# Performance work log

Measured on AMD Instinct MI355X. Metric: run time of the kernel, lower is better.

The kernel has to match this reference:

```python
import jax, jax.numpy as jnp
import numpy as np

EPS = 1e-5

def binarize(x):
    # straight-through-estimator sign binarization (identity gradient),
    # matching the torch .data-mutation trick in BinarizeConv2d/BinarizeLinear
    return x + jax.lax.stop_gradient(jnp.sign(x) - x)

def conv3x3(x, w, b):
    # NCHW conv, stride 1, padding 1, binarized weights, float bias
    y = jax.lax.conv_general_dilated(x, binarize(w), window_strides=(1, 1),
                                     padding=((1, 1), (1, 1)),
                                     dimension_numbers=('NCHW', 'OIHW', 'NCHW'))
    return y + b[None, :, None, None]

def maxpool2(x):
    return jax.lax.reduce_window(x, -jnp.inf, jax.lax.max,
                                 (1, 1, 2, 2), (1, 1, 2, 2), 'VALID')

def bn2d(x, g, b):
    # training-mode batchnorm (batch statistics)
    m = jnp.mean(x, axis=(0, 2, 3), keepdims=True)
    v = jnp.var(x, axis=(0, 2, 3), keepdims=True)
    return (x - m) * jax.lax.rsqrt(v + EPS) * g[None, :, None, None] + b[None, :, None, None]

def bn1d(x, g, b):
    m = jnp.mean(x, axis=0)
    v = jnp.var(x, axis=0)
    return (x - m) * jax.lax.rsqrt(v + EPS) * g + b

def htanh(x):
    return jnp.clip(x, -1.0, 1.0)


def setup_inputs() -> dict:
    key = jax.random.key(0)
    ks = jax.random.split(key, 16)
    B = 1024
    inp = {
        'x':   jax.random.normal(ks[0], (B, 1, 28, 28), jnp.float32),
        'w1':  jax.random.normal(ks[1], (48, 1, 3, 3), jnp.float32) * 0.1,
        'b1':  jnp.zeros((48,), jnp.float32),
        'g1':  jnp.ones((48,), jnp.float32),  'be1': jnp.zeros((48,), jnp.float32),
        'w2':  jax.random.normal(ks[2], (128, 48, 3, 3), jnp.float32) * 0.05,
        'b2':  jnp.zeros((128,), jnp.float32),
        'g2':  jnp.ones((128,), jnp.float32), 'be2': jnp.zeros((128,), jnp.float32),
        'w3':  jax.random.normal(ks[3], (256, 128, 3, 3), jnp.float32) * 0.03,
        'b3':  jnp.zeros((256,), jnp.float32),
        'g3':  jnp.ones((256,), jnp.float32), 'be3': jnp.zeros((256,), jnp.float32),
        'wf1': jax.random.normal(ks[4], (2048, 256 * 7 * 7), jnp.float32) * 0.01,
        'bf1': jnp.zeros((2048,), jnp.float32),
        'g4':  jnp.ones((2048,), jnp.float32), 'be4': jnp.zeros((2048,), jnp.float32),
        'wf2': jax.random.normal(ks[5], (10, 2048), jnp.float32) * 0.02,
        'bf2': jnp.zeros((10,), jnp.float32),
    }
    return inp


def reference(x, w1, b1, g1, be1, w2, b2, g2, be2, w3, b3, g3, be3,
              wf1, bf1, g4, be4, wf2, bf2):
    # features
    h = conv3x3(binarize(x), w1, b1)          # [B,48,28,28] (input binarized: C=1 != 3)
    h = maxpool2(h)                            # [B,48,14,14]
    h = htanh(bn2d(h, g1, be1))
    h = conv3x3(binarize(h), w2, b2)          # [B,128,14,14]
    h = htanh(bn2d(h, g2, be2))
    h = conv3x3(binarize(h), w3, b3)          # [B,256,14,14]
    h = maxpool2(h)                            # [B,256,7,7]
    h = htanh(bn2d(h, g3, be3))
    # classifier
    h = h.reshape(-1, 256 * 7 * 7)
    h = binarize(h) @ binarize(wf1).T + bf1    # [B,2048]
    h = htanh(bn1d(h, g4, be4))
    # Dropout(0.5) is identity in eval mode
    h = h @ wf2.T + bf2                        # [B,10]
    return jax.nn.log_softmax(h, axis=1)
```

## Files before the change

### kernel.cpp

```cpp
#include <hip/hip_runtime.h>
#include <math.h>

typedef __attribute__((ext_vector_type(8))) short short8;
typedef __attribute__((ext_vector_type(4))) float f32x4;
typedef unsigned short ushort_t;

#define B_    1024
#define EPSV  1e-5

__device__ __forceinline__ float sgn(float v){ return (v>0.f)?1.f:((v<0.f)?-1.f:0.f); }
__device__ __forceinline__ ushort_t sgnbits(float v){ return (v>0.f)?(ushort_t)0x3F80:((v<0.f)?(ushort_t)0xBF80:(ushort_t)0); }

__global__ __launch_bounds__(256) void k_conv1_pool(const float* __restrict__ x,
                                                    const float* __restrict__ w1,
                                                    float* __restrict__ p1){
  int idx = blockIdx.x*256 + threadIdx.x;
  if (idx >= B_*196*64) return;
  int c = idx & 63;
  int p = (idx >> 6) % 196;
  int b = (idx >> 6) / 196;
  if (c >= 48){ p1[idx] = 0.f; return; }
  int y = p/14, xq = p - y*14;
  const float* xb = x + (size_t)b*784;
  float w[9];
#pragma unroll
  for (int k=0;k<9;k++) w[k] = sgn(w1[c*9+k]);
  float sx[4][4];
#pragma unroll
  for (int dy=0; dy<4; dy++){
    int iy = 2*y-1+dy;
#pragma unroll
    for (int dx=0; dx<4; dx++){
      int ix = 2*xq-1+dx;
      sx[dy][dx] = (iy>=0 && iy<28 && ix>=0 && ix<28) ? sgn(xb[iy*28+ix]) : 0.f;
    }
  }
  float best = -1e30f;
#pragma unroll
  for (int py=0;py<2;py++)
#pragma unroll
    for (int px=0;px<2;px++){
      float acc = 0.f;
#pragma unroll
      for (int ky=0;ky<3;ky++)
#pragma unroll
        for (int kx=0;kx<3;kx++)
          acc += sx[py+ky][px+kx]*w[ky*3+kx];
      best = fmaxf(best, acc);
    }
  p1[idx] = best;
}

__global__ __launch_bounds__(256) void k_stats_cols(const float* __restrict__ src,
                                                    double* __restrict__ sum,
                                                    double* __restrict__ sumsq,
                                                    int C, long rows){
  int c = blockIdx.x*256 + threadIdx.x;
  if (c >= C) return;
  double a=0.0, a2=0.0;
  for (long r = blockIdx.y; r < rows; r += gridDim.y){
    double v = (double)src[r*(long)C + c];
    a += v; a2 += v*v;
  }
  atomicAdd(&sum[c], a); atomicAdd(&sumsq[c], a2);
}

__global__ __launch_bounds__(256) void k_stats_cf(const float* __restrict__ src,
                                                  double* __restrict__ sum,
                                                  double* __restrict__ sumsq,
                                                  int Bn, int C, int S){
  int c = blockIdx.x;
  long NS = (long)Bn*S;
  double a=0.0, a2=0.0;
  long stride = (long)gridDim.y*blockDim.x;
  for (long i = (long)blockIdx.y*blockDim.x + threadIdx.x; i < NS; i += stride){
    long b = i / S, s = i - b*S;
    double v = (double)src[((size_t)b*C + c)*S + s];
    a += v; a2 += v*v;
  }
  __shared__ double rs[256], rs2[256];
  rs[threadIdx.x]=a; rs2[threadIdx.x]=a2;
  __syncthreads();
  for (int off=128; off>0; off>>=1){
    if (threadIdx.x < off){ rs[threadIdx.x]+=rs[threadIdx.x+off]; rs2[threadIdx.x]+=rs2[threadIdx.x+off]; }
    __syncthreads();
  }
  if (threadIdx.x==0){ atomicAdd(&sum[c], rs[0]); atomicAdd(&sumsq[c], rs2[0]); }
}

__global__ void k_bnparams(const double* __restrict__ sum, const double* __restrict__ sumsq,
                           const float* __restrict__ g, const float* __restrict__ be,
                           float* __restrict__ scale, float* __restrict__ shift,
                           int C, int validC, double invN){
  int c = blockIdx.x*blockDim.x + threadIdx.x;
  if (c >= C) return;
  if (c >= validC){ scale[c]=0.f; shift[c]=0.f; return; }
  double m   = sum[c]*invN;
  double var = sumsq[c]*invN - m*m;
  double s   = (double)g[c] / sqrt(var + EPSV);
  scale[c] = (float)s;
  shift[c] = (float)((double)be[c] - m*s);
}

__global__ __launch_bounds__(256) void k_norm_sign(const float* __restrict__ src,
                                                   ushort_t* __restrict__ dst,
                                                   const float* __restrict__ scale,
                                                   const float* __restrict__ shift,
                                                   int C, int S, int total){
  int i = blockIdx.x*256 + threadIdx.x;
  if (i >= total) return;
  int c = (i / S) % C;
  float v = fmaf(src[i], scale[c], shift[c]);
  dst[i] = sgnbits(v);
}

__global__ __launch_bounds__(256) void k_norm_htanh(float* __restrict__ buf,
                                                    const float* __restrict__ scale,
                                                    const float* __restrict__ shift,
                                                    int C, int total){
  int i = blockIdx.x*256 + threadIdx.x;
  if (i >= total) return;
  int c = i % C;
  float v = fmaf(buf[i], scale[c], shift[c]);
  buf[i] = fminf(fmaxf(v,-1.f),1.f);
}

__global__ __launch_bounds__(256) void k_prep_w2(const float* __restrict__ w2, ushort_t* __restrict__ out){
  int idx = blockIdx.x*256 + threadIdx.x;
  if (idx >= 128*576) return;
  int oc = idx / 576, r = idx - oc*576;
  int kk = r >> 6, ic = r & 63;
  out[idx] = (ic < 48) ? sgnbits(w2[oc*432 + ic*9 + kk]) : (ushort_t)0;
}
__global__ __launch_bounds__(256) void k_prep_w3(const float* __restrict__ w3, ushort_t* __restrict__ out){
  int idx = blockIdx.x*256 + threadIdx.x;
  if (idx >= 256*1152) return;
  int oc = idx / 1152, r = idx - oc*1152;
  int kk = r >> 7, ic = r & 127;
  out[idx] = sgnbits(w3[oc*1152 + ic*9 + kk]);
}
__global__ __launch_bounds__(256) void k_prep_wf1(const float* __restrict__ wf1, ushort_t* __restrict__ out){
  int idx = blockIdx.x*256 + threadIdx.x;
  if (idx >= 2048*12544/4) return;
  const float4 v = *reinterpret_cast<const float4*>(&wf1[(size_t)idx*4]);
  ushort4 o;
  o.x = sgnbits(v.x); o.y = sgnbits(v.y); o.z = sgnbits(v.z); o.w = sgnbits(v.w);
  *reinterpret_cast<ushort4*>(&out[(size_t)idx*4]) = o;
}

__global__ __launch_bounds__(256,2) void k_conv2_mfma(const ushort_t* __restrict__ a1,
                                                      const ushort_t* __restrict__ w2b,
                                                      float* __restrict__ c2){
  __shared__ ushort_t sIn[256*64];
  __shared__ ushort_t sW[2][64*40];
  int ocb = blockIdx.x*64;
  int b   = blockIdx.y;
  int tid = threadIdx.x;
  {
    const uint4* src4 = reinterpret_cast<const uint4*>(a1 + (size_t)b*196*64);
    for (int i = tid; i < 2048; i += 256){
      int px = i >> 3, ch = i & 7;
      int py = px >> 4, pxx = px & 15;
      uint4 v = make_uint4(0u,0u,0u,0u);
      if (py>=1 && py<=14 && pxx>=1 && pxx<=14)
        v = src4[((py-1)*14 + (pxx-1))*8 + ch];
      *reinterpret_cast<uint4*>(&sIn[px*64 + ((ch ^ (px & 7))<<3)]) = v;
    }
  }
  const uint4* wsrc = reinterpret_cast<const uint4*>(w2b);
  int ocS = ocb + (tid>>2), kcS = tid & 3;
  *reinterpret_cast<uint4*>(&sW[0][(tid>>2)*40 + kcS*8]) = wsrc[(size_t)ocS*72 + kcS];
  __syncthreads();

  int lane = tid & 63, wave = tid >> 6;
  int rA = lane & 15, kch = lane >> 4;
  f32x4 acc[4][4];
#pragma unroll
  for (int t=0;t<4;t++)
#pragma unroll
    for (int n=0;n<4;n++) acc[t][n] = (f32x4){0.f,0.f,0.f,0.f};

  for (int s = 0; s < 18; ++s){
    int cur = s & 1;
    uint4 wpre;
    if (s < 17) wpre = wsrc[(size_t)ocS*72 + (s+1)*4 + kcS];
    short8 bF[4];
#pragma unroll
    for (int n=0;n<4;n++)
      bF[n] = *reinterpret_cast<const short8*>(&sW[cur][(n*16+rA)*40 + kch*8]);
    int kk9 = s >> 1;
    int ky = kk9/3, kx = kk9 - ky*3;
    int chbase = ((s & 1) << 2) + kch;
#pragma unroll
    for (int t=0;t<4;t++){
      int m = t*4 + wave;
      if (m < 13){
        int r = m*16 + rA;
        int rc = r < 196 ? r : 195;
        int y = rc/14, x = rc - y*14;
        int px = (y+ky)*16 + (x+kx);
        short8 aF = *reinterpret_cast<const short8*>(&sIn[px*64 + ((chbase ^ (px&7))<<3)]);
#pragma unroll
        for (int n=0;n<4;n++)
          acc[t][n] = __builtin_amdgcn_mfma_f32_16x16x32_bf16(aF, bF[n], acc[t][n], 0,0,0);
      }
    }
    if (s < 17) *reinterpret_cast<uint4*>(&sW[cur^1][(tid>>2)*40 + kcS*8]) = wpre;
    __syncthreads();
  }
  int colL = lane & 15, rg = lane >> 4;
#pragma unroll
  for (int t=0;t<4;t++){
    int m = t*4 + wave;
    if (m < 13){
#pragma unroll
      for (int n=0;n<4;n++)
#pragma unroll
        for (int j=0;j<4;j++){
          int r = m*16 + rg*4 + j;
          if (r < 196)
            c2[((size_t)b*196 + r)*128 + ocb + n*16 + colL] = acc[t][n][j];
        }
    }
  }
}

__global__ __launch_bounds__(256,2) void k_conv3_mfma_pool(const ushort_t* __restrict__ a2,
                                                           const ushort_t* __restrict__ w3b,
                                                           float* __restrict__ p3){
  __shared__ ushort_t sIn[256*128];
  __shared__ ushort_t sW[2][64*40];
  int ocb = blockIdx.x*64;
  int b   = blockIdx.y;
  int tid = threadIdx.x;
  {
    const uint4* src4 = reinterpret_cast<const uint4*>(a2 + (size_t)b*196*128);
    for (int i = tid; i < 4096; i += 256){
      int px = i >> 4, ch = i & 15;
      int py = px >> 4, pxx = px & 15;
      uint4 v = make_uint4(0u,0u,0u,0u);
      if (py>=1 && py<=14 && pxx>=1 && pxx<=14)
        v = src4[((py-1)*14 + (pxx-1))*16 + ch];
      *reinterpret_cast<uint4*>(&sIn[px*128 + ((ch ^ (px & 15))<<3)]) = v;
    }
  }
  const uint4* wsrc = reinterpret_cast<const uint4*>(w3b);
  int ocS = ocb + (tid>>2), kcS = tid & 3;
  *reinterpret_cast<uint4*>(&sW[0][(tid>>2)*40 + kcS*8]) = wsrc[(size_t)ocS*144 + kcS];
  __syncthreads();

  int lane = tid & 63, wave = tid >> 6;
  int rA = lane & 15, kch = lane >> 4;
  f32x4 acc[4][4];
#pragma unroll
  for (int t=0;t<4;t++)
#pragma unroll
    for (int n=0;n<4;n++) acc[t][n] = (f32x4){0.f,0.f,0.f,0.f};

  for (int s = 0; s < 36; ++s){
    int cur = s & 1;
    uint4 wpre;
    if (s < 35) wpre = wsrc[(size_t)ocS*144 + (s+1)*4 + kcS];
    short8 bF[4];
#pragma unroll
    for (int n=0;n<4;n++)
      bF[n] = *reinterpret_cast<const short8*>(&sW[cur][(n*16+rA)*40 + kch*8]);
    int kk9 = s >> 2;
    int ky = kk9/3, kx = kk9 - ky*3;
    int chbase = ((s & 3) << 2) + kch;
#pragma unroll
    for (int t=0;t<4;t++){
      int m = t*4 + wave;
      if (m < 13){
        int r = m*16 + rA;
        int rc = r < 196 ? r : 195;
        int y = rc/14, x = rc - y*14;
        int px = (y+ky)*16 + (x+kx);
        short8 aF = *reinterpret_cast<const short8*>(&sIn[px*128 + ((chbase ^ (px&15))<<3)]);
#pragma unroll
        for (int n=0;n<4;n++)
          acc[t][n] = __builtin_amdgcn_mfma_f32_16x16x32_bf16(aF, bF[n], acc[t][n], 0,0,0);
      }
    }
    if (s < 35) *reinterpret_cast<uint4*>(&sW[cur^1][(tid>>2)*40 + kcS*8]) = wpre;
    __syncthreads();
  }
  float* sPool = reinterpret_cast<float*>(sIn);
  int colL = lane & 15, rg = lane >> 4;
#pragma unroll
  for (int t=0;t<4;t++){
    int m = t*4 + wave;
    if (m < 13){
#pragma unroll
      for (int n=0;n<4;n++)
#pragma unroll
        for (int j=0;j<4;j++){
          int r = m*16 + rg*4 + j;
          if (r < 196) sPool[(n*16+colL)*212 + r] = acc[t][n][j];
        }
    }
  }
  __syncthreads();
  for (int i = tid; i < 64*49; i += 256){
    int oc = i/49, cell = i - oc*49;
    int cy = cell/7, cx = cell - cy*7;
    const float* rp = &sPool[oc*212 + cy*28 + cx*2];
    float m0 = fmaxf(rp[0],  rp[1]);
    float m1 = fmaxf(rp[14], rp[15]);
    p3[((size_t)b*256 + ocb + oc)*49 + cell] = fmaxf(m0, m1);
  }
}

__global__ __launch_bounds__(256) void k_fc1_mfma(const ushort_t* __restrict__ A,
                                                  const ushort_t* __restrict__ Bw,
                                                  float* __restrict__ f1){
  __shared__ ushort_t As[2][64*40];
  __shared__ ushort_t Bs[2][128*40];
  int bn = blockIdx.x*128, bm = blockIdx.y*64;
  int tid = threadIdx.x;
  int rS = tid >> 2, kcS = tid & 3;
  {
    *reinterpret_cast<uint4*>(&As[0][rS*40 + kcS*8]) =
      *reinterpret_cast<const uint4*>(&A[(size_t)(bm+rS)*12544 + kcS*8]);
    *reinterpret_cast<uint4*>(&Bs[0][rS*40 + kcS*8]) =
      *reinterpret_cast<const uint4*>(&Bw[(size_t)(bn+rS)*12544 + kcS*8]);
    *reinterpret_cast<uint4*>(&Bs[0][(64+rS)*40 + kcS*8]) =
      *reinterpret_cast<const uint4*>(&Bw[(size_t)(bn+64+rS)*12544 + kcS*8]);
  }
  __syncthreads();
  int lane = tid & 63, wave = tid >> 6;
  int rA = lane & 15, kch = lane >> 4;
  int mtb = (wave & 1)*2, ntb = (wave >> 1)*4;
  f32x4 acc[2][4];
#pragma unroll
  for (int i=0;i<2;i++)
#pragma unroll
    for (int n=0;n<4;n++) acc[i][n] = (f32x4){0.f,0.f,0.f,0.f};

  for (int s = 0; s < 392; ++s){
    int cur = s & 1;
    uint4 pa, pb0, pb1;
    if (s < 391){
      size_t k0 = (size_t)(s+1)*32 + kcS*8;
      pa  = *reinterpret_cast<const uint4*>(&A [(size_t)(bm+rS)*12544 + k0]);
      pb0 = *reinterpret_cast<const uint4*>(&Bw[(size_t)(bn+rS)*12544 + k0]);
      pb1 = *reinterpret_cast<const uint4*>(&Bw[(size_t)(bn+64+rS)*12544 + k0]);
    }
    short8 aF[2], bF[4];
#pragma unroll
    for (int i=0;i<2;i++)
      aF[i] = *reinterpret_cast<const short8*>(&As[cur][((mtb+i)*16+rA)*40 + kch*8]);
#pragma unroll
    for (int n=0;n<4;n++)
      bF[n] = *reinterpret_cast<const short8*>(&Bs[cur][((ntb+n)*16+rA)*40 + kch*8]);
#pragma unroll
    for (int i=0;i<2;i++)
#pragma unroll
      for (int n=0;n<4;n++)
        acc[i][n] = __builtin_amdgcn_mfma_f32_16x16x32_bf16(aF[i], bF[n], acc[i][n], 0,0,0);
    if (s < 391){
      *reinterpret_cast<uint4*>(&As[cur^1][rS*40 + kcS*8]) = pa;
      *reinterpret_cast<uint4*>(&Bs[cur^1][rS*40 + kcS*8]) = pb0;
      *reinterpret_cast<uint4*>(&Bs[cur^1][(64+rS)*40 + kcS*8]) = pb1;
    }
    __syncthreads();
  }
  int colL = lane & 15, rg = lane >> 4;
#pragma unroll
  for (int i=0;i<2;i++)
#pragma unroll
    for (int n=0;n<4;n++)
#pragma unroll
      for (int j=0;j<4;j++){
        int r = bm + (mtb+i)*16 + rg*4 + j;
        int col = bn + (ntb+n)*16 + colL;
        f1[(size_t)r*2048 + col] = acc[i][n][j];
      }
}

__global__ __launch_bounds__(256) void k_fc2_lsm(const float* __restrict__ h,
                                                 const float* __restrict__ W,
                                                 const float* __restrict__ bias,
                                                 float* __restrict__ out){
  int b = blockIdx.x;
  const float* hb = h + (size_t)b*2048;
  float acc[10];
#pragma unroll
  for (int o=0;o<10;o++) acc[o]=0.f;
  for (int k=threadIdx.x; k<2048; k+=256){
    float v = hb[k];
#pragma unroll
    for (int o=0;o<10;o++) acc[o] += v*W[o*2048+k];
  }
  __shared__ float red[4][10];
  int wv = threadIdx.x>>6, lanev = threadIdx.x&63;
#pragma unroll
  for (int o=0;o<10;o++){
    float r = acc[o];
    for (int off=32; off>0; off>>=1) r += __shfl_down(r, off);
    if (lanev==0) red[wv][o]=r;
  }
  __syncthreads();
  if (threadIdx.x==0){
    float lg[10], mx=-1e30f;
#pragma unroll
    for (int o=0;o<10;o++){ lg[o]=red[0][o]+red[1][o]+red[2][o]+red[3][o]+bias[o]; mx=fmaxf(mx,lg[o]); }
    float se=0.f;
#pragma unroll
    for (int o=0;o<10;o++) se += expf(lg[o]-mx);
    float lse = mx + logf(se);
#pragma unroll
    for (int o=0;o<10;o++) out[(size_t)b*10+o] = lg[o]-lse;
  }
}

extern "C" void kernel_launch(void* const* d_in, const int* in_sizes, int n_in,
                              void* d_out, int out_size, void* d_ws, size_t ws_size,
                              hipStream_t stream){
  (void)in_sizes; (void)n_in; (void)out_size; (void)ws_size;
  const float* x   = (const float*)d_in[0];
  const float* w1  = (const float*)d_in[1];
  const float* g1  = (const float*)d_in[3];
  const float* be1 = (const float*)d_in[4];
  const float* w2  = (const float*)d_in[5];
  const float* g2  = (const float*)d_in[7];
  const float* be2 = (const float*)d_in[8];
  const float* w3  = (const float*)d_in[9];
  const float* g3  = (const float*)d_in[11];
  const float* be3 = (const float*)d_in[12];
  const float* wf1 = (const float*)d_in[13];
  const float* g4  = (const float*)d_in[15];
  const float* be4 = (const float*)d_in[16];
  const float* wf2 = (const float*)d_in[17];
  const float* bf2 = (const float*)d_in[18];
  float* out = (float*)d_out;

  char* W = (char*)d_ws;
  double* sum   = (double*)W;
  double* sumsq = sum + 2048;
  float*  scale = (float*)(W + 32768);
  float*  shift = scale + 2048;
  float*    p1   = (float*)   (W + 65536);
  float*    c2   = (float*)   (W + 65536);
  float*    p3   = (float*)   (W + 65536);
  ushort_t* a3   = (ushort_t*)(W + 51445760);
  ushort_t* wf1b = (ushort_t*)(W + 77135872);
  ushort_t* a1   = (ushort_t*)(W + 102825984);
  ushort_t* w2b  = (ushort_t*)(W + 128516096);
  ushort_t* a2   = (ushort_t*)(W + 128663552);
  ushort_t* w3b  = (ushort_t*)(W + 180043776);
  float*    f1   = (float*)   (W + 180633600);

  k_conv1_pool<<<50176, 256, 0, stream>>>(x, w1, p1);
  hipMemsetAsync(sum, 0, 32768, stream);
  k_stats_cols<<<dim3(1,512), 256, 0, stream>>>(p1, sum, sumsq, 64, 200704L);
  k_bnparams<<<1, 256, 0, stream>>>(sum, sumsq, g1, be1, scale, shift, 64, 48, 1.0/200704.0);
  k_norm_sign<<<50176, 256, 0, stream>>>(p1, a1, scale, shift, 64, 1, 12845056);
  k_prep_w2<<<288, 256, 0, stream>>>(w2, w2b);
  k_conv2_mfma<<<dim3(2, B_), 256, 0, stream>>>(a1, w2b, c2);
  hipMemsetAsync(sum, 0, 32768, stream);
  k_stats_cols<<<dim3(1,512), 256, 0, stream>>>(c2, sum, sumsq, 128, 200704L);
  k_bnparams<<<1, 256, 0, stream>>>(sum, sumsq, g2, be2, scale, shift, 128, 128, 1.0/200704.0);
  k_norm_sign<<<100352, 256, 0, stream>>>(c2, a2, scale, shift, 128, 1, 25690112);
  k_prep_wf1<<<25088, 256, 0, stream>>>(wf1, wf1b);
  k_prep_w3<<<1152, 256, 0, stream>>>(w3, w3b);
  k_conv3_mfma_pool<<<dim3(4, B_), 256, 0, stream>>>(a2, w3b, p3);
  hipMemsetAsync(sum, 0, 32768, stream);
  k_stats_cf<<<dim3(256,16), 256, 0, stream>>>(p3, sum, sumsq, B_, 256, 49);
  k_bnparams<<<1, 256, 0, stream>>>(sum, sumsq, g3, be3, scale, shift, 256, 256, 1.0/50176.0);
  k_norm_sign<<<50176, 256, 0, stream>>>(p3, a3, scale, shift, 256, 49, 12845056);
  k_fc1_mfma<<<dim3(16,16), 256, 0, stream>>>(a3, wf1b, f1);
  hipMemsetAsync(sum, 0, 32768, stream);
  k_stats_cols<<<dim3(8,64), 256, 0, stream>>>(f1, sum, sumsq, 2048, 1024L);
  k_bnparams<<<8, 256, 0, stream>>>(sum, sumsq, g4, be4, scale, shift, 2048, 2048, 1.0/1024.0);
  k_norm_htanh<<<8192, 256, 0, stream>>>(f1, scale, shift, 2048, 2097152);
  k_fc2_lsm<<<B_, 256, 0, stream>>>(f1, wf2, bf2, out);
}
```

Measured before the change: 1.084 ms.

## Fuse BN statistics into conv/fc epilogues and widen MFMA tiles

Conv2, conv3 and fc1 now accumulate per-channel sum and sum-of-squares in their epilogues and write per-block partials. A small reduce kernel combines them, replacing the separate passes that re-read c2, p3 and f1. Conv2 computes all 128 output channels per block, and conv3 uses 128-channel tiles that stage input channels in two halves of shared memory. The fc1 K-step doubles to 64 with swizzled shared layouts, and the first BN stats kernel uses a 4-row-per-block layout. Partial sums are fp32 before the double reduction, which slightly changes precision, and the larger accumulator tiles raise register pressure.

```diff
diff --git a/kernel.cpp b/kernel.cpp
--- a/kernel.cpp
+++ b/kernel.cpp
@@ -10,6 +10,9 @@
 
 __device__ __forceinline__ float sgn(float v){ return (v>0.f)?1.f:((v<0.f)?-1.f:0.f); }
 __device__ __forceinline__ ushort_t sgnbits(float v){ return (v>0.f)?(ushort_t)0x3F80:((v<0.f)?(ushort_t)0xBF80:(ushort_t)0); }
+
+#define SWZW(o,c) ( ((o)<<6) ^ ((((c) ^ ((o)&7)) & 7) << 4) )
+#define SWZF(o,c) ( ((o)<<7) + ((((c) ^ ((o)&7)) & 7) << 4) )
 
 __global__ __launch_bounds__(256) void k_conv1_pool(const float* __restrict__ x,
                                                     const float* __restrict__ w1,
@@ -51,41 +54,42 @@
   p1[idx] = best;
 }
 
-__global__ __launch_bounds__(256) void k_stats_cols(const float* __restrict__ src,
+__global__ __launch_bounds__(256) void k_stats_cl64(const float* __restrict__ src,
                                                     double* __restrict__ sum,
                                                     double* __restrict__ sumsq,
-                                                    int C, long rows){
+                                                    long rows){
+  int c = threadIdx.x & 63, sl = threadIdx.x >> 6;
+  double a=0.0, q=0.0;
+  long stride = (long)gridDim.y*4;
+  for (long r = (long)blockIdx.y*4 + sl; r < rows; r += stride){
+    double v = (double)src[r*64 + c];
+    a += v; q += v*v;
+  }
+  __shared__ double sA[256], sQd[256];
+  sA[threadIdx.x]=a; sQd[threadIdx.x]=q;
+  __syncthreads();
+  if (threadIdx.x < 64){
+    a = sA[threadIdx.x] + sA[threadIdx.x+64] + sA[threadIdx.x+128] + sA[threadIdx.x+192];
+    q = sQd[threadIdx.x] + sQd[threadIdx.x+64] + sQd[threadIdx.x+128] + sQd[threadIdx.x+192];
+    atomicAdd(&sum[c], a); atomicAdd(&sumsq[c], q);
+  }
+}
+
+__global__ __launch_bounds__(256) void k_reduce_stats(const float* __restrict__ pS,
+                                                      const float* __restrict__ pQ,
+                                                      double* __restrict__ sum,
+                                                      double* __restrict__ sumsq,
+                                                      int C, int nPart){
   int c = blockIdx.x*256 + threadIdx.x;
   if (c >= C) return;
-  double a=0.0, a2=0.0;
-  for (long r = blockIdx.y; r < rows; r += gridDim.y){
-    double v = (double)src[r*(long)C + c];
-    a += v; a2 += v*v;
-  }
-  atomicAdd(&sum[c], a); atomicAdd(&sumsq[c], a2);
-}
-
-__global__ __launch_bounds__(256) void k_stats_cf(const float* __restrict__ src,
-                                                  double* __restrict__ sum,
-                                                  double* __restrict__ sumsq,
-                                                  int Bn, int C, int S){
-  int c = blockIdx.x;
-  long NS = (long)Bn*S;
-  double a=0.0, a2=0.0;
-  long stride = (long)gridDim.y*blockDim.x;
-  for (long i = (long)blockIdx.y*blockDim.x + threadIdx.x; i < NS; i += stride){
-    long b = i / S, s = i - b*S;
-    double v = (double)src[((size_t)b*C + c)*S + s];
-    a += v; a2 += v*v;
-  }
-  __shared__ double rs[256], rs2[256];
-  rs[threadIdx.x]=a; rs2[threadIdx.x]=a2;
-  __syncthreads();
-  for (int off=128; off>0; off>>=1){
-    if (threadIdx.x < off){ rs[threadIdx.x]+=rs[threadIdx.x+off]; rs2[threadIdx.x]+=rs2[threadIdx.x+off]; }
-    __syncthreads();
-  }
-  if (threadIdx.x==0){ atomicAdd(&sum[c], rs[0]); atomicAdd(&sumsq[c], rs2[0]); }
+  int per = (nPart + gridDim.y - 1)/gridDim.y;
+  int p0 = blockIdx.y*per, p1 = p0+per; if (p1 > nPart) p1 = nPart;
+  double a=0.0, q=0.0;
+  for (int p = p0; p < p1; ++p){
+    a += (double)pS[(size_t)p*C + c];
+    q += (double)pQ[(size_t)p*C + c];
+  }
+  atomicAdd(&sum[c], a); atomicAdd(&sumsq[c], q);
 }
 
 __global__ void k_bnparams(const double* __restrict__ sum, const double* __restrict__ sumsq,
@@ -150,12 +154,13 @@
 
 __global__ __launch_bounds__(256,2) void k_conv2_mfma(const ushort_t* __restrict__ a1,
                                                       const ushort_t* __restrict__ w2b,
-                                                      float* __restrict__ c2){
+                                                      float* __restrict__ c2,
+                                                      float* __restrict__ pS,
+                                                      float* __restrict__ pQ){
   __shared__ ushort_t sIn[256*64];
-  __shared__ ushort_t sW[2][64*40];
-  int ocb = blockIdx.x*64;
-  int b   = blockIdx.y;
-  int tid = threadIdx.x;
+  __shared__ char     sWb[2][8192];
+  __shared__ float    sRS[128], sRQ[128];
+  int b = blockIdx.x, tid = threadIdx.x;
   {
     const uint4* src4 = reinterpret_cast<const uint4*>(a1 + (size_t)b*196*64);
     for (int i = tid; i < 2048; i += 256){
@@ -167,27 +172,37 @@
       *reinterpret_cast<uint4*>(&sIn[px*64 + ((ch ^ (px & 7))<<3)]) = v;
     }
   }
-  const uint4* wsrc = reinterpret_cast<const uint4*>(w2b);
-  int ocS = ocb + (tid>>2), kcS = tid & 3;
-  *reinterpret_cast<uint4*>(&sW[0][(tid>>2)*40 + kcS*8]) = wsrc[(size_t)ocS*72 + kcS];
-  __syncthreads();
-
+  if (tid < 128){ sRS[tid]=0.f; sRQ[tid]=0.f; }
+  const uint4* gW = reinterpret_cast<const uint4*>(w2b);
+  int cS = tid & 3, rS = (tid >> 2)*2;
+  {
+    uint4 v0 = gW[(size_t)rS*72 + cS];
+    uint4 v1 = gW[(size_t)(rS+1)*72 + cS];
+    *reinterpret_cast<uint4*>(&sWb[0][SWZW(rS,  cS)]) = v0;
+    *reinterpret_cast<uint4*>(&sWb[0][SWZW(rS+1,cS)]) = v1;
+  }
+  __syncthreads();
   int lane = tid & 63, wave = tid >> 6;
   int rA = lane & 15, kch = lane >> 4;
-  f32x4 acc[4][4];
+  f32x4 acc[4][8];
 #pragma unroll
   for (int t=0;t<4;t++)
 #pragma unroll
-    for (int n=0;n<4;n++) acc[t][n] = (f32x4){0.f,0.f,0.f,0.f};
+    for (int n=0;n<8;n++) acc[t][n] = (f32x4){0.f,0.f,0.f,0.f};
 
   for (int s = 0; s < 18; ++s){
     int cur = s & 1;
-    uint4 wpre;
-    if (s < 17) wpre = wsrc[(size_t)ocS*72 + (s+1)*4 + kcS];
-    short8 bF[4];
-#pragma unroll
-    for (int n=0;n<4;n++)
-      bF[n] = *reinterpret_cast<const short8*>(&sW[cur][(n*16+rA)*40 + kch*8]);
+    uint4 w0, w1;
+    if (s < 17){
+      w0 = gW[(size_t)rS*72 + (s+1)*4 + cS];
+      w1 = gW[(size_t)(rS+1)*72 + (s+1)*4 + cS];
+    }
+    short8 bF[8];
+#pragma unroll
+    for (int n=0;n<8;n++){
+      int o = n*16 + rA;
+      bF[n] = *reinterpret_cast<const short8*>(&sWb[cur][SWZW(o, kch)]);
+    }
     int kk9 = s >> 1;
     int ky = kk9/3, kx = kk9 - ky*3;
     int chbase = ((s & 1) << 2) + kch;
@@ -201,73 +216,110 @@
         int px = (y+ky)*16 + (x+kx);
         short8 aF = *reinterpret_cast<const short8*>(&sIn[px*64 + ((chbase ^ (px&7))<<3)]);
 #pragma unroll
-        for (int n=0;n<4;n++)
+        for (int n=0;n<8;n++)
           acc[t][n] = __builtin_amdgcn_mfma_f32_16x16x32_bf16(aF, bF[n], acc[t][n], 0,0,0);
       }
     }
-    if (s < 17) *reinterpret_cast<uint4*>(&sW[cur^1][(tid>>2)*40 + kcS*8]) = wpre;
+    if (s < 17){
+      *reinterpret_cast<uint4*>(&sWb[cur^1][SWZW(rS,  cS)]) = w0;
+      *reinterpret_cast<uint4*>(&sWb[cur^1][SWZW(rS+1,cS)]) = w1;
+    }
     __syncthreads();
   }
   int colL = lane & 15, rg = lane >> 4;
+  float csum[8], csq[8];
+#pragma unroll
+  for (int n=0;n<8;n++){ csum[n]=0.f; csq[n]=0.f; }
 #pragma unroll
   for (int t=0;t<4;t++){
     int m = t*4 + wave;
     if (m < 13){
 #pragma unroll
-      for (int n=0;n<4;n++)
+      for (int n=0;n<8;n++)
 #pragma unroll
         for (int j=0;j<4;j++){
           int r = m*16 + rg*4 + j;
-          if (r < 196)
-            c2[((size_t)b*196 + r)*128 + ocb + n*16 + colL] = acc[t][n][j];
+          if (r < 196){
+            float v = acc[t][n][j];
+            c2[((size_t)b*196 + r)*128 + n*16 + colL] = v;
+            csum[n] += v; csq[n] += v*v;
+          }
         }
     }
+  }
+#pragma unroll
+  for (int n=0;n<8;n++){
+    float a = csum[n], q = csq[n];
+    a += __shfl_down(a,32); a += __shfl_down(a,16);
+    q += __shfl_down(q,32); q += __shfl_down(q,16);
+    if (rg == 0){
+      atomicAdd(&sRS[n*16+colL], a);
+      atomicAdd(&sRQ[n*16+colL], q);
+    }
+  }
+  __syncthreads();
+  if (tid < 128){
+    pS[(size_t)b*128 + tid] = sRS[tid];
+    pQ[(size_t)b*128 + tid] = sRQ[tid];
   }
 }
 
 __global__ __launch_bounds__(256,2) void k_conv3_mfma_pool(const ushort_t* __restrict__ a2,
                                                            const ushort_t* __restrict__ w3b,
-                                                           float* __restrict__ p3){
-  __shared__ ushort_t sIn[256*128];
-  __shared__ ushort_t sW[2][64*40];
-  int ocb = blockIdx.x*64;
+                                                           float* __restrict__ p3,
+                                                           float* __restrict__ pS,
+                                                           float* __restrict__ pQ){
+  __shared__ ushort_t sIn[256*64];
+  __shared__ char     sWb[2][8192];
+  __shared__ float    sS[32], sQ[32];
+  int ocb = blockIdx.x*128;
   int b   = blockIdx.y;
   int tid = threadIdx.x;
+  const uint4* src4 = reinterpret_cast<const uint4*>(a2 + (size_t)b*196*128);
+  for (int i = tid; i < 2048; i += 256){
+    int px = i >> 3, ch = i & 7;
+    int py = px >> 4, pxx = px & 15;
+    uint4 v = make_uint4(0u,0u,0u,0u);
+    if (py>=1 && py<=14 && pxx>=1 && pxx<=14)
+      v = src4[((py-1)*14 + (pxx-1))*16 + ch];
+    *reinterpret_cast<uint4*>(&sIn[px*64 + ((ch ^ (px & 7))<<3)]) = v;
+  }
+  const uint4* gW = reinterpret_cast<const uint4*>(w3b);
+  int cS = tid & 3, rS = (tid >> 2)*2;
   {
-    const uint4* src4 = reinterpret_cast<const uint4*>(a2 + (size_t)b*196*128);
-    for (int i = tid; i < 4096; i += 256){
-      int px = i >> 4, ch = i & 15;
-      int py = px >> 4, pxx = px & 15;
-      uint4 v = make_uint4(0u,0u,0u,0u);
-      if (py>=1 && py<=14 && pxx>=1 && pxx<=14)
-        v = src4[((py-1)*14 + (pxx-1))*16 + ch];
-      *reinterpret_cast<uint4*>(&sIn[px*128 + ((ch ^ (px & 15))<<3)]) = v;
-    }
-  }
-  const uint4* wsrc = reinterpret_cast<const uint4*>(w3b);
-  int ocS = ocb + (tid>>2), kcS = tid & 3;
-  *reinterpret_cast<uint4*>(&sW[0][(tid>>2)*40 + kcS*8]) = wsrc[(size_t)ocS*144 + kcS];
-  __syncthreads();
-
+    uint4 v0 = gW[(size_t)(ocb+rS)*144 + cS];
+    uint4 v1 = gW[(size_t)(ocb+rS+1)*144 + cS];
+    *reinterpret_cast<uint4*>(&sWb[0][SWZW(rS,  cS)]) = v0;
+    *reinterpret_cast<uint4*>(&sWb[0][SWZW(rS+1,cS)]) = v1;
+  }
+  __syncthreads();
   int lane = tid & 63, wave = tid >> 6;
   int rA = lane & 15, kch = lane >> 4;
-  f32x4 acc[4][4];
+  f32x4 acc[4][8];
 #pragma unroll
   for (int t=0;t<4;t++)
 #pragma unroll
-    for (int n=0;n<4;n++) acc[t][n] = (f32x4){0.f,0.f,0.f,0.f};
+    for (int n=0;n<8;n++) acc[t][n] = (f32x4){0.f,0.f,0.f,0.f};
 
   for (int s = 0; s < 36; ++s){
     int cur = s & 1;
-    uint4 wpre;
-    if (s < 35) wpre = wsrc[(size_t)ocS*144 + (s+1)*4 + kcS];
-    short8 bF[4];
-#pragma unroll
-    for (int n=0;n<4;n++)
-      bF[n] = *reinterpret_cast<const short8*>(&sW[cur][(n*16+rA)*40 + kch*8]);
-    int kk9 = s >> 2;
+    uint4 w0, w1;
+    if (s < 35){
+      int s1 = s+1; int h1 = (s1 >= 18); int sl1 = s1 - h1*18;
+      int wofs = (sl1>>1)*16 + h1*8 + (sl1&1)*4;
+      w0 = gW[(size_t)(ocb+rS)*144 + wofs + cS];
+      w1 = gW[(size_t)(ocb+rS+1)*144 + wofs + cS];
+    }
+    short8 bF[8];
+#pragma unroll
+    for (int n=0;n<8;n++){
+      int o = n*16 + rA;
+      bF[n] = *reinterpret_cast<const short8*>(&sWb[cur][SWZW(o, kch)]);
+    }
+    int h = (s >= 18); int sloc = s - h*18;
+    int kk9 = sloc >> 1;
     int ky = kk9/3, kx = kk9 - ky*3;
-    int chbase = ((s & 3) << 2) + kch;
+    int chbase = ((sloc & 1) << 2) + kch;
 #pragma unroll
     for (int t=0;t<4;t++){
       int m = t*4 + wave;
@@ -276,106 +328,165 @@
         int rc = r < 196 ? r : 195;
         int y = rc/14, x = rc - y*14;
         int px = (y+ky)*16 + (x+kx);
-        short8 aF = *reinterpret_cast<const short8*>(&sIn[px*128 + ((chbase ^ (px&15))<<3)]);
-#pragma unroll
-        for (int n=0;n<4;n++)
+        short8 aF = *reinterpret_cast<const short8*>(&sIn[px*64 + ((chbase ^ (px&7))<<3)]);
+#pragma unroll
+        for (int n=0;n<8;n++)
           acc[t][n] = __builtin_amdgcn_mfma_f32_16x16x32_bf16(aF, bF[n], acc[t][n], 0,0,0);
       }
     }
-    if (s < 35) *reinterpret_cast<uint4*>(&sW[cur^1][(tid>>2)*40 + kcS*8]) = wpre;
-    __syncthreads();
+    if (s < 35){
+      *reinterpret_cast<uint4*>(&sWb[cur^1][SWZW(rS,  cS)]) = w0;
+      *reinterpret_cast<uint4*>(&sWb[cur^1][SWZW(rS+1,cS)]) = w1;
+    }
+    if (s == 17){
+      __syncthreads();
+      for (int i = tid; i < 2048; i += 256){
+        int px = i >> 3, ch = i & 7;
+        int py = px >> 4, pxx = px & 15;
+        uint4 v = make_uint4(0u,0u,0u,0u);
+        if (py>=1 && py<=14 && pxx>=1 && pxx<=14)
+          v = src4[((py-1)*14 + (pxx-1))*16 + 8 + ch];
+        *reinterpret_cast<uint4*>(&sIn[px*64 + ((ch ^ (px & 7))<<3)]) = v;
+      }
+      __syncthreads();
+    } else {
+      __syncthreads();
+    }
   }
   float* sPool = reinterpret_cast<float*>(sIn);
   int colL = lane & 15, rg = lane >> 4;
-#pragma unroll
-  for (int t=0;t<4;t++){
-    int m = t*4 + wave;
-    if (m < 13){
-#pragma unroll
-      for (int n=0;n<4;n++)
-#pragma unroll
-        for (int j=0;j<4;j++){
-          int r = m*16 + rg*4 + j;
-          if (r < 196) sPool[(n*16+colL)*212 + r] = acc[t][n][j];
+  for (int q = 0; q < 4; ++q){
+    __syncthreads();
+#pragma unroll
+    for (int t=0;t<4;t++){
+      int m = t*4 + wave;
+      if (m < 13){
+#pragma unroll
+        for (int nl=0;nl<2;nl++){
+          int n = q*2 + nl;
+#pragma unroll
+          for (int j=0;j<4;j++){
+            int r = m*16 + rg*4 + j;
+            if (r < 196) sPool[(nl*16+colL)*197 + r] = acc[t][n][j];
+          }
         }
-    }
-  }
-  __syncthreads();
-  for (int i = tid; i < 64*49; i += 256){
-    int oc = i/49, cell = i - oc*49;
-    int cy = cell/7, cx = cell - cy*7;
-    const float* rp = &sPool[oc*212 + cy*28 + cx*2];
-    float m0 = fmaxf(rp[0],  rp[1]);
-    float m1 = fmaxf(rp[14], rp[15]);
-    p3[((size_t)b*256 + ocb + oc)*49 + cell] = fmaxf(m0, m1);
-  }
-}
-
-__global__ __launch_bounds__(256) void k_fc1_mfma(const ushort_t* __restrict__ A,
-                                                  const ushort_t* __restrict__ Bw,
-                                                  float* __restrict__ f1){
-  __shared__ ushort_t As[2][64*40];
-  __shared__ ushort_t Bs[2][128*40];
-  int bn = blockIdx.x*128, bm = blockIdx.y*64;
+      }
+    }
+    if (tid < 32){ sS[tid]=0.f; sQ[tid]=0.f; }
+    __syncthreads();
+    for (int i = tid; i < 32*49; i += 256){
+      int oc = i/49, cell = i - oc*49;
+      int cy = cell/7, cx = cell - cy*7;
+      const float* rp = &sPool[oc*197 + cy*28 + cx*2];
+      float v = fmaxf(fmaxf(rp[0],rp[1]), fmaxf(rp[14],rp[15]));
+      p3[((size_t)b*256 + ocb + q*32 + oc)*49 + cell] = v;
+      atomicAdd(&sS[oc], v); atomicAdd(&sQ[oc], v*v);
+    }
+    __syncthreads();
+    if (tid < 32){
+      pS[(size_t)b*256 + ocb + q*32 + tid] = sS[tid];
+      pQ[(size_t)b*256 + ocb + q*32 + tid] = sQ[tid];
+    }
+  }
+}
+
+__global__ __launch_bounds__(256,2) void k_fc1_mfma(const ushort_t* __restrict__ A,
+                                                    const ushort_t* __restrict__ Bw,
+                                                    float* __restrict__ f1,
+                                                    float* __restrict__ pS,
+                                                    float* __restrict__ pQ){
+  __shared__ char As[2][8192];
+  __shared__ char Bs[2][16384];
+  __shared__ float sCS[128], sCQ[128];
+  int id = blockIdx.x;
+  int bm = (id & 15) << 6, bn = (id >> 4) << 7;
   int tid = threadIdx.x;
-  int rS = tid >> 2, kcS = tid & 3;
+  int cS = tid & 7;
+  int rS = tid >> 3;
+  const uint4* gA = reinterpret_cast<const uint4*>(A);
+  const uint4* gB = reinterpret_cast<const uint4*>(Bw);
   {
-    *reinterpret_cast<uint4*>(&As[0][rS*40 + kcS*8]) =
-      *reinterpret_cast<const uint4*>(&A[(size_t)(bm+rS)*12544 + kcS*8]);
-    *reinterpret_cast<uint4*>(&Bs[0][rS*40 + kcS*8]) =
-      *reinterpret_cast<const uint4*>(&Bw[(size_t)(bn+rS)*12544 + kcS*8]);
-    *reinterpret_cast<uint4*>(&Bs[0][(64+rS)*40 + kcS*8]) =
-      *reinterpret_cast<const uint4*>(&Bw[(size_t)(bn+64+rS)*12544 + kcS*8]);
-  }
+    *reinterpret_cast<uint4*>(&As[0][SWZF(rS,   cS)]) = gA[(size_t)(bm+rS   )*1568 + cS];
+    *reinterpret_cast<uint4*>(&As[0][SWZF(rS+32,cS)]) = gA[(size_t)(bm+rS+32)*1568 + cS];
+#pragma unroll
+    for (int j=0;j<4;j++)
+      *reinterpret_cast<uint4*>(&Bs[0][SWZF(rS+j*32,cS)]) = gB[(size_t)(bn+rS+j*32)*1568 + cS];
+  }
+  if (tid < 128){ sCS[tid]=0.f; sCQ[tid]=0.f; }
   __syncthreads();
   int lane = tid & 63, wave = tid >> 6;
   int rA = lane & 15, kch = lane >> 4;
-  int mtb = (wave & 1)*2, ntb = (wave >> 1)*4;
+  int wm = wave & 1, wn = wave >> 1;
   f32x4 acc[2][4];
 #pragma unroll
   for (int i=0;i<2;i++)
 #pragma unroll
     for (int n=0;n<4;n++) acc[i][n] = (f32x4){0.f,0.f,0.f,0.f};
 
-  for (int s = 0; s < 392; ++s){
+  for (int s = 0; s < 196; ++s){
     int cur = s & 1;
-    uint4 pa, pb0, pb1;
-    if (s < 391){
-      size_t k0 = (size_t)(s+1)*32 + kcS*8;
-      pa  = *reinterpret_cast<const uint4*>(&A [(size_t)(bm+rS)*12544 + k0]);
-      pb0 = *reinterpret_cast<const uint4*>(&Bw[(size_t)(bn+rS)*12544 + k0]);
-      pb1 = *reinterpret_cast<const uint4*>(&Bw[(size_t)(bn+64+rS)*12544 + k0]);
-    }
-    short8 aF[2], bF[4];
+    uint4 pa0, pa1, pb[4];
+    if (s < 195){
+      size_t k0 = (size_t)(s+1)*8 + cS;
+      pa0 = gA[(size_t)(bm+rS   )*1568 + k0];
+      pa1 = gA[(size_t)(bm+rS+32)*1568 + k0];
+#pragma unroll
+      for (int j=0;j<4;j++)
+        pb[j] = gB[(size_t)(bn+rS+j*32)*1568 + k0];
+    }
+#pragma unroll
+    for (int u = 0; u < 2; ++u){
+      short8 aF[2], bF[4];
+#pragma unroll
+      for (int i=0;i<2;i++){
+        int ro = wm*32 + i*16 + rA;
+        aF[i] = *reinterpret_cast<const short8*>(&As[cur][SWZF(ro, u*4+kch)]);
+      }
+#pragma unroll
+      for (int n=0;n<4;n++){
+        int co = wn*64 + n*16 + rA;
+        bF[n] = *reinterpret_cast<const short8*>(&Bs[cur][SWZF(co, u*4+kch)]);
+      }
+#pragma unroll
+      for (int i=0;i<2;i++)
+#pragma unroll
+        for (int n=0;n<4;n++)
+          acc[i][n] = __builtin_amdgcn_mfma_f32_16x16x32_bf16(aF[i], bF[n], acc[i][n], 0,0,0);
+    }
+    if (s < 195){
+      *reinterpret_cast<uint4*>(&As[cur^1][SWZF(rS,   cS)]) = pa0;
+      *reinterpret_cast<uint4*>(&As[cur^1][SWZF(rS+32,cS)]) = pa1;
+#pragma unroll
+      for (int j=0;j<4;j++)
+        *reinterpret_cast<uint4*>(&Bs[cur^1][SWZF(rS+j*32,cS)]) = pb[j];
+    }
+    __syncthreads();
+  }
+  int colL = lane & 15, rg = lane >> 4;
+#pragma unroll
+  for (int n=0;n<4;n++){
+    float ls = 0.f, lq = 0.f;
 #pragma unroll
     for (int i=0;i<2;i++)
-      aF[i] = *reinterpret_cast<const short8*>(&As[cur][((mtb+i)*16+rA)*40 + kch*8]);
-#pragma unroll
-    for (int n=0;n<4;n++)
-      bF[n] = *reinterpret_cast<const short8*>(&Bs[cur][((ntb+n)*16+rA)*40 + kch*8]);
-#pragma unroll
-    for (int i=0;i<2;i++)
-#pragma unroll
-      for (int n=0;n<4;n++)
-        acc[i][n] = __builtin_amdgcn_mfma_f32_16x16x32_bf16(aF[i], bF[n], acc[i][n], 0,0,0);
-    if (s < 391){
-      *reinterpret_cast<uint4*>(&As[cur^1][rS*40 + kcS*8]) = pa;
-      *reinterpret_cast<uint4*>(&Bs[cur^1][rS*40 + kcS*8]) = pb0;
-      *reinterpret_cast<uint4*>(&Bs[cur^1][(64+rS)*40 + kcS*8]) = pb1;
-    }
-    __syncthreads();
-  }
-  int colL = lane & 15, rg = lane >> 4;
-#pragma unroll
-  for (int i=0;i<2;i++)
-#pragma unroll
-    for (int n=0;n<4;n++)
 #pragma unroll
       for (int j=0;j<4;j++){
-        int r = bm + (mtb+i)*16 + rg*4 + j;
-        int col = bn + (ntb+n)*16 + colL;
-        f1[(size_t)r*2048 + col] = acc[i][n][j];
-      }
+        int r = bm + wm*32 + i*16 + rg*4 + j;
+        float v = acc[i][n][j];
+        f1[(size_t)r*2048 + bn + wn*64 + n*16 + colL] = v;
+        ls += v; lq += v*v;
+      }
+    ls += __shfl_down(ls,32); ls += __shfl_down(ls,16);
+    lq += __shfl_down(lq,32); lq += __shfl_down(lq,16);
+    if (rg == 0){
+      atomicAdd(&sCS[wn*64 + n*16 + colL], ls);
+      atomicAdd(&sCQ[wn*64 + n*16 + colL], lq);
+    }
+  }
+  __syncthreads();
+  if (tid < 128){
+    pS[(size_t)(id&15)*2048 + bn + tid] = sCS[tid];
+    pQ[(size_t)(id&15)*2048 + bn + tid] = sCQ[tid];
+  }
 }
 
 __global__ __launch_bounds__(256) void k_fc2_lsm(const float* __restrict__ h,
@@ -443,35 +554,41 @@
   float*    p1   = (float*)   (W + 65536);
   float*    c2   = (float*)   (W + 65536);
   float*    p3   = (float*)   (W + 65536);
+  float*    f1   = (float*)   (W + 65536);
   ushort_t* a3   = (ushort_t*)(W + 51445760);
   ushort_t* wf1b = (ushort_t*)(W + 77135872);
   ushort_t* a1   = (ushort_t*)(W + 102825984);
   ushort_t* w2b  = (ushort_t*)(W + 128516096);
   ushort_t* a2   = (ushort_t*)(W + 128663552);
   ushort_t* w3b  = (ushort_t*)(W + 180043776);
-  float*    f1   = (float*)   (W + 180633600);
+  float*    pS2  = (float*)   (W + 180633600);
+  float*    pQ2  = pS2 + 131072;
+  float*    pS3  = pQ2 + 131072;
+  float*    pQ3  = pS3 + 262144;
+  float*    pSF  = pQ3 + 262144;
+  float*    pQF  = pSF + 32768;
 
   k_conv1_pool<<<50176, 256, 0, stream>>>(x, w1, p1);
   hipMemsetAsync(sum, 0, 32768, stream);
-  k_stats_cols<<<dim3(1,512), 256, 0, stream>>>(p1, sum, sumsq, 64, 200704L);
+  k_stats_cl64<<<dim3(1,128), 256, 0, stream>>>(p1, sum, sumsq, 200704L);
   k_bnparams<<<1, 256, 0, stream>>>(sum, sumsq, g1, be1, scale, shift, 64, 48, 1.0/200704.0);
   k_norm_sign<<<50176, 256, 0, stream>>>(p1, a1, scale, shift, 64, 1, 12845056);
   k_prep_w2<<<288, 256, 0, stream>>>(w2, w2b);
-  k_conv2_mfma<<<dim3(2, B_), 256, 0, stream>>>(a1, w2b, c2);
+  k_prep_w3<<<1152, 256, 0, stream>>>(w3, w3b);
+  k_conv2_mfma<<<1024, 256, 0, stream>>>(a1, w2b, c2, pS2, pQ2);
   hipMemsetAsync(sum, 0, 32768, stream);
-  k_stats_cols<<<dim3(1,512), 256, 0, stream>>>(c2, sum, sumsq, 128, 200704L);
+  k_reduce_stats<<<dim3(1,32), 256, 0, stream>>>(pS2, pQ2, sum, sumsq, 128, 1024);
   k_bnparams<<<1, 256, 0, stream>>>(sum, sumsq, g2, be2, scale, shift, 128, 128, 1.0/200704.0);
   k_norm_sign<<<100352, 256, 0, stream>>>(c2, a2, scale, shift, 128, 1, 25690112);
   k_prep_wf1<<<25088, 256, 0, stream>>>(wf1, wf1b);
-  k_prep_w3<<<1152, 256, 0, stream>>>(w3, w3b);
-  k_conv3_mfma_pool<<<dim3(4, B_), 256, 0, stream>>>(a2, w3b, p3);
+  k_conv3_mfma_pool<<<dim3(2, B_), 256, 0, stream>>>(a2, w3b, p3, pS3, pQ3);
   hipMemsetAsync(sum, 0, 32768, stream);
-  k_stats_cf<<<dim3(256,16), 256, 0, stream>>>(p3, sum, sumsq, B_, 256, 49);
+  k_reduce_stats<<<dim3(1,32), 256, 0, stream>>>(pS3, pQ3, sum, sumsq, 256, 1024);
   k_bnparams<<<1, 256, 0, stream>>>(sum, sumsq, g3, be3, scale, shift, 256, 256, 1.0/50176.0);
   k_norm_sign<<<50176, 256, 0, stream>>>(p3, a3, scale, shift, 256, 49, 12845056);
-  k_fc1_mfma<<<dim3(16,16), 256, 0, stream>>>(a3, wf1b, f1);
+  k_fc1_mfma<<<256, 256, 0, stream>>>(a3, wf1b, f1, pSF, pQF);
   hipMemsetAsync(sum, 0, 32768, stream);
-  k_stats_cols<<<dim3(8,64), 256, 0, stream>>>(f1, sum, sumsq, 2048, 1024L);
+  k_reduce_stats<<<dim3(8,1), 256, 0, stream>>>(pSF, pQF, sum, sumsq, 2048, 16);
   k_bnparams<<<8, 256, 0, stream>>>(sum, sumsq, g4, be4, scale, shift, 2048, 2048, 1.0/1024.0);
   k_norm_htanh<<<8192, 256, 0, stream>>>(f1, scale, shift, 2048, 2097152);
   k_fc2_lsm<<<B_, 256, 0, stream>>>(f1, wf2, bf2, out);
```

New measurement: 1.077 ms. No clear change (-0.6%).
